# Optimization experiments

Measured on AMD Instinct MI355X. Metric: run time of the kernel, lower is better.

## Reference

```python
import jax, jax.numpy as jnp
import numpy as np

N_EMBD = 768
N_HEAD = 12
HEAD_SIZE = N_EMBD // N_HEAD
LN_EPS = 1e-5


def setup_inputs() -> dict:
    key = jax.random.key(0)
    ks = jax.random.split(key, 12)
    s = 0.02
    B, T, C = 8, 1024, N_EMBD
    return {
        "x":  jax.random.normal(ks[0], (B, T, C), dtype=jnp.float32),
        # per-head q/k/v projections packed as [C, H*hs] (concat of head outputs)
        "Wq": jax.random.normal(ks[1], (C, C), dtype=jnp.float32) * s,
        "Wk": jax.random.normal(ks[2], (C, C), dtype=jnp.float32) * s,
        "Wv": jax.random.normal(ks[3], (C, C), dtype=jnp.float32) * s,
        "Wo": jax.random.normal(ks[4], (C, C), dtype=jnp.float32) * s,
        "bo": jnp.zeros((C,), dtype=jnp.float32),
        "W1": jax.random.normal(ks[5], (C, 4 * C), dtype=jnp.float32) * s,
        "b1": jnp.zeros((4 * C,), dtype=jnp.float32),
        "W2": jax.random.normal(ks[6], (4 * C, C), dtype=jnp.float32) * s,
        "b2": jnp.zeros((C,), dtype=jnp.float32),
        "g1": jnp.ones((C,), dtype=jnp.float32),
        "be1": jnp.zeros((C,), dtype=jnp.float32),
        "g2": jnp.ones((C,), dtype=jnp.float32),
        "be2": jnp.zeros((C,), dtype=jnp.float32),
    }


def _layernorm(x, g, b):
    mu = jnp.mean(x, axis=-1, keepdims=True)
    var = jnp.mean(jnp.square(x - mu), axis=-1, keepdims=True)
    return (x - mu) * jax.lax.rsqrt(var + LN_EPS) * g + b


def _block(x, Wq, Wk, Wv, Wo, bo, W1, b1, W2, b2, g1, be1, g2, be2):
    B, T, C = x.shape
    H, hs = N_HEAD, HEAD_SIZE
    h = _layernorm(x, g1, be1)
    q = (h @ Wq).reshape(B, T, H, hs)
    k = (h @ Wk).reshape(B, T, H, hs)
    v = (h @ Wv).reshape(B, T, H, hs)
    # NOTE: original code scales by n_embd**-0.5 (C from x.shape), not head_size**-0.5
    scores = jnp.einsum("bthd,bshd->bhts", q, k) * (C ** -0.5)
    causal = jnp.tril(jnp.ones((T, T), dtype=bool))  # [T,T]
    scores = jnp.where(causal, scores, -jnp.inf)
    attn = jax.nn.softmax(scores, axis=-1)  # [B,H,T,T]
    o = jnp.einsum("bhts,bshd->bthd", attn, v).reshape(B, T, C)
    x = x + o @ Wo + bo
    h2 = _layernorm(x, g2, be2)
    ff = jax.nn.gelu(h2 @ W1 + b1, approximate=False) @ W2 + b2
    return x + ff


def reference(x, Wq, Wk, Wv, Wo, bo, W1, b1, W2, b2, g1, be1, g2, be2):
    return _block(x, Wq, Wk, Wv, Wo, bo, W1, b1, W2, b2, g1, be1, g2, be2)
```

## Files before the change

kernel.cpp:

```cpp
#include <hip/hip_runtime.h>
#include <math.h>
#include <stdint.h>

typedef unsigned short u16;
typedef unsigned int u32;
typedef __attribute__((ext_vector_type(8))) __bf16 bf16x8;
typedef __attribute__((ext_vector_type(4))) float f32x4;

#define AS1 __attribute__((address_space(1)))
#define AS3 __attribute__((address_space(3)))

__device__ __forceinline__ void stage16(const void* g, void* l) {
    __builtin_amdgcn_global_load_lds((const AS1 void*)(uintptr_t)g,
                                     (AS3 void*)(uintptr_t)l, 16, 0, 0);
}

__device__ __forceinline__ u16 f2bf(float f) {
    u32 u = __float_as_uint(f);
    u += 0x7fffu + ((u >> 16) & 1u);
    return (u16)(u >> 16);
}

__global__ __launch_bounds__(256) void ln_kernel(const float* __restrict__ x,
                                                 const float* __restrict__ g,
                                                 const float* __restrict__ b,
                                                 u16* __restrict__ out) {
    int row = blockIdx.x;
    int tid = threadIdx.x;
    const float* xr = x + (size_t)row * 768;
    float x0 = xr[tid], x1 = xr[tid + 256], x2 = xr[tid + 512];

    __shared__ float red[256];
    red[tid] = x0 + x1 + x2;
    __syncthreads();
    for (int off = 128; off > 0; off >>= 1) {
        if (tid < off) red[tid] += red[tid + off];
        __syncthreads();
    }
    float mu = red[0] * (1.0f / 768.0f);
    __syncthreads();

    float d0 = x0 - mu, d1 = x1 - mu, d2 = x2 - mu;
    red[tid] = d0 * d0 + d1 * d1 + d2 * d2;
    __syncthreads();
    for (int off = 128; off > 0; off >>= 1) {
        if (tid < off) red[tid] += red[tid + off];
        __syncthreads();
    }
    float var = red[0] * (1.0f / 768.0f);
    float rs = rsqrtf(var + 1e-5f);

    u16* orow = out + (size_t)row * 768;
    orow[tid]       = f2bf(d0 * rs * g[tid]       + b[tid]);
    orow[tid + 256] = f2bf(d1 * rs * g[tid + 256] + b[tid + 256]);
    orow[tid + 512] = f2bf(d2 * rs * g[tid + 512] + b[tid + 512]);
}

__global__ __launch_bounds__(256) void transpose_bf16(const float* __restrict__ W,
                                                      u16* __restrict__ Wt,
                                                      int K, int N) {
    __shared__ float t[32][33];
    int tx = threadIdx.x, ty = threadIdx.y;
    int n0 = blockIdx.x * 32, k0 = blockIdx.y * 32;
#pragma unroll
    for (int j = 0; j < 32; j += 8)
        t[ty + j][tx] = W[(size_t)(k0 + ty + j) * N + n0 + tx];
    __syncthreads();
#pragma unroll
    for (int j = 0; j < 32; j += 8)
        Wt[(size_t)(n0 + ty + j) * K + k0 + tx] = f2bf(t[tx][ty + j]);
}

__global__ __launch_bounds__(256) void vt_kernel(const u16* __restrict__ qkv,
                                                 u16* __restrict__ Vt) {
    __shared__ u16 t[32][34];
    const int tx = threadIdx.x, ty = threadIdx.y;
    const int s0 = blockIdx.x * 32, d0 = blockIdx.y * 32, bh = blockIdx.z;
    const int b = bh / 12, h = bh % 12;
#pragma unroll
    for (int j = 0; j < 32; j += 8)
        t[ty + j][tx] = qkv[((size_t)(b * 1024) + s0 + ty + j) * 2304 + 1536 + h * 64 + d0 + tx];
    __syncthreads();
#pragma unroll
    for (int j = 0; j < 32; j += 8)
        Vt[((size_t)bh * 64 + d0 + ty + j) * 1024 + s0 + tx] = t[tx][ty + j];
}

__global__ __launch_bounds__(256, 3) void gemm_k32(
    const u16* __restrict__ A, const u16* __restrict__ Bt,
    const float* __restrict__ bias, const float* __restrict__ res,
    float* __restrict__ outF, u16* __restrict__ outB,
    int N, int K, int act) {
    __shared__ char lds[49152];
    const int tid = threadIdx.x, lane = tid & 63, wid = tid >> 6;
    const int l15 = lane & 15, lk = lane >> 4;
    const int wrow = (wid >> 1) * 64, wcol = (wid & 1) * 64;

    int wg = blockIdx.y * gridDim.x + blockIdx.x;
    const int nwg = gridDim.x * gridDim.y;
    wg = (wg & 7) * (nwg >> 3) + (wg >> 3);
    const int brow = (wg / gridDim.x) * 128;
    const int bcol = (wg % gridDim.x) * 128;

    const size_t K2 = (size_t)K * 2;
    const char* Abase = (const char*)A + (size_t)brow * K2;
    const char* Bbase = (const char*)Bt + (size_t)bcol * K2;

    int srow[2], scol[2];
#pragma unroll
    for (int j = 0; j < 2; ++j) {
        const int L = j * 4096 + tid * 16;
        srow[j] = L >> 6;
        scol[j] = (L & 63) ^ (((srow[j] >> 1) & 3) << 4);
    }

    const int nt = K >> 5;

    auto stage_tile = [&](int t, char* dst) {
#pragma unroll
        for (int j = 0; j < 2; ++j) {
            const size_t off = (size_t)srow[j] * K2 + (size_t)t * 64 + scol[j];
            stage16(Abase + off, dst + j * 4096 + tid * 16);
            stage16(Bbase + off, dst + 8192 + j * 4096 + tid * 16);
        }
    };

    f32x4 acc[4][4] = {};

    stage_tile(0, lds);
    stage_tile(1, lds + 16384);

    for (int t = 0; t < nt; ++t) {
        if (t + 1 < nt) asm volatile("s_waitcnt vmcnt(4)\n\ts_barrier" ::: "memory");
        else            asm volatile("s_waitcnt vmcnt(0)\n\ts_barrier" ::: "memory");
        __builtin_amdgcn_sched_barrier(0);

        if (t + 2 < nt) stage_tile(t + 2, lds + ((t + 2) % 3) * 16384);

        const char* As = lds + (t % 3) * 16384;
        const char* Bs = As + 8192;
        bf16x8 af[4], bfv[4];
#pragma unroll
        for (int m = 0; m < 4; ++m) {
            const int row = wrow + m * 16 + l15;
            af[m] = *(const bf16x8*)(As + row * 64 +
                                     ((lk * 16) ^ (((row >> 1) & 3) << 4)));
        }
#pragma unroll
        for (int n = 0; n < 4; ++n) {
            const int row = wcol + n * 16 + l15;
            bfv[n] = *(const bf16x8*)(Bs + row * 64 +
                                      ((lk * 16) ^ (((row >> 1) & 3) << 4)));
        }
        __builtin_amdgcn_s_setprio(1);
#pragma unroll
        for (int m = 0; m < 4; ++m)
#pragma unroll
            for (int n = 0; n < 4; ++n)
                acc[m][n] = __builtin_amdgcn_mfma_f32_16x16x32_bf16(af[m], bfv[n], acc[m][n], 0, 0, 0);
        __builtin_amdgcn_s_setprio(0);
    }

#pragma unroll
    for (int m = 0; m < 4; ++m)
#pragma unroll
        for (int n = 0; n < 4; ++n)
#pragma unroll
            for (int r = 0; r < 4; ++r) {
                int row = brow + wrow + m * 16 + lk * 4 + r;
                int col = bcol + wcol + n * 16 + l15;
                float v = acc[m][n][r];
                if (bias) v += bias[col];
                if (act) v = 0.5f * v * (1.0f + erff(v * 0.70710678118654752f));
                if (res) v += res[(size_t)row * N + col];
                if (outB) outB[(size_t)row * N + col] = f2bf(v);
                else outF[(size_t)row * N + col] = v;
            }
}

__global__ __launch_bounds__(256) void attn_mfma(const u16* __restrict__ qkv,
                                                 const u16* __restrict__ Vt,
                                                 u16* __restrict__ obf) {
    __shared__ char lds[40960];
    const int tid = threadIdx.x, lane = tid & 63, w = tid >> 6;
    const int g = lane >> 4, l15 = lane & 15;

    int wg = blockIdx.y * gridDim.x + blockIdx.x;
    const int nwg = gridDim.x * gridDim.y;
    wg = (wg & 7) * (nwg >> 3) + (wg >> 3);
    const int qb = 15 - (wg & 15);
    const int bh = wg >> 4;
    const int h = bh % 12, b = bh / 12;
    const int t0 = qb * 64;
    const float scale = 0.03608439182435161f;

    const size_t qrow = ((size_t)b * 1024 + t0 + 16 * w + l15) * 2304 + h * 64;
    const bf16x8 qf0 = *(const bf16x8*)(qkv + qrow + 8 * g);
    const bf16x8 qf1 = *(const bf16x8*)(qkv + qrow + 8 * g + 32);

    const int sub = ((lane & 7) * 16) ^ ((lane >> 3) << 4);
    const int r0 = 16 * w + (lane >> 3);
    const char* kSrc = (const char*)qkv + ((size_t)(b * 1024 + r0) * 2304 + 768 + h * 64) * 2 + sub;
    const char* vSrc = (const char*)Vt + ((size_t)(bh * 64 + r0) * 1024) * 2 + sub;
    const int dstOff = 2 * w * 1024 + lane * 16;

    stage16(kSrc,            lds + dstOff);
    stage16(kSrc + 8 * 4608, lds + dstOff + 1024);
    stage16(vSrc,            lds + 8192 + dstOff);
    stage16(vSrc + 8 * 2048, lds + 8192 + dstOff + 1024);
    kSrc += 64 * 4608; vSrc += 128;
    __syncthreads();

    const int swzA = (l15 & 7) << 4;
    float m_r[4] = {-1e30f, -1e30f, -1e30f, -1e30f};
    float l_r[4] = {0.f, 0.f, 0.f, 0.f};
    f32x4 oacc[4] = {};
    char* Pw = lds + 32768 + w * 2048;

    for (int c = 0; c <= qb; ++c) {
        if (c < qb) {
            char* dst = lds + ((c + 1) & 1) * 16384;
            stage16(kSrc,            dst + dstOff);
            stage16(kSrc + 8 * 4608, dst + dstOff + 1024);
            stage16(vSrc,            dst + 8192 + dstOff);
            stage16(vSrc + 8 * 2048, dst + 8192 + dstOff + 1024);
            kSrc += 64 * 4608; vSrc += 128;
            asm volatile("s_waitcnt vmcnt(4)\n\ts_barrier" ::: "memory");
        } else {
            asm volatile("s_waitcnt vmcnt(0)\n\ts_barrier" ::: "memory");
        }
        __builtin_amdgcn_sched_barrier(0);

        const char* bufK = lds + (c & 1) * 16384;
        const char* bufV = bufK + 8192;

        f32x4 sacc[4] = {};
#pragma unroll
        for (int st = 0; st < 4; ++st) {
            const char* krow = bufK + (l15 + 16 * st) * 128;
            const bf16x8 kf0 = *(const bf16x8*)(krow + ((16 * g) ^ swzA));
            const bf16x8 kf1 = *(const bf16x8*)(krow + ((16 * g + 64) ^ swzA));
            sacc[st] = __builtin_amdgcn_mfma_f32_16x16x32_bf16(qf0, kf0, sacc[st], 0, 0, 0);
            sacc[st] = __builtin_amdgcn_mfma_f32_16x16x32_bf16(qf1, kf1, sacc[st], 0, 0, 0);
        }

        const bool diag = (c == qb);
#pragma unroll
        for (int r = 0; r < 4; ++r) {
            float sv0 = sacc[0][r] * scale, sv1 = sacc[1][r] * scale;
            float sv2 = sacc[2][r] * scale, sv3 = sacc[3][r] * scale;
            if (diag) {
                const int trel = 16 * w + 4 * g + r;
                if (l15 +  0 > trel) sv0 = -1e30f;
                if (l15 + 16 > trel) sv1 = -1e30f;
                if (l15 + 32 > trel) sv2 = -1e30f;
                if (l15 + 48 > trel) sv3 = -1e30f;
            }
            float mx = fmaxf(fmaxf(sv0, sv1), fmaxf(sv2, sv3));
#pragma unroll
            for (int off = 1; off < 16; off <<= 1) mx = fmaxf(mx, __shfl_xor(mx, off));
            const float mnew = fmaxf(m_r[r], mx);
            const float corr = __expf(m_r[r] - mnew);
            const float p0 = __expf(sv0 - mnew), p1 = __expf(sv1 - mnew);
            const float p2 = __expf(sv2 - mnew), p3 = __expf(sv3 - mnew);
            float ps = p0 + p1 + p2 + p3;
#pragma unroll
            for (int off = 1; off < 16; off <<= 1) ps += __shfl_xor(ps, off);
            l_r[r] = l_r[r] * corr + ps;
            m_r[r] = mnew;
            oacc[0][r] *= corr; oacc[1][r] *= corr;
            oacc[2][r] *= corr; oacc[3][r] *= corr;
            const int q = 4 * g + r;
            char* pr = Pw + q * 128;
            const int sw = (q & 7) << 4;
            *(u16*)(pr + ((l15 * 2 +  0) ^ sw)) = f2bf(p0);
            *(u16*)(pr + ((l15 * 2 + 32) ^ sw)) = f2bf(p1);
            *(u16*)(pr + ((l15 * 2 + 64) ^ sw)) = f2bf(p2);
            *(u16*)(pr + ((l15 * 2 + 96) ^ sw)) = f2bf(p3);
        }

#pragma unroll
        for (int kc = 0; kc < 2; ++kc) {
            const bf16x8 pa = *(const bf16x8*)(Pw + l15 * 128 + ((16 * g + 64 * kc) ^ swzA));
#pragma unroll
            for (int dt = 0; dt < 4; ++dt) {
                const int d = l15 + 16 * dt;
                const bf16x8 vf = *(const bf16x8*)(bufV + d * 128 +
                                   ((16 * g + 64 * kc) ^ ((d & 7) << 4)));
                oacc[dt] = __builtin_amdgcn_mfma_f32_16x16x32_bf16(pa, vf, oacc[dt], 0, 0, 0);
            }
        }
        asm volatile("s_barrier" ::: "memory");
    }

    const size_t orow0 = ((size_t)b * 1024 + t0 + 16 * w) * 768 + h * 64;
#pragma unroll
    for (int r = 0; r < 4; ++r) {
        const float inv = 1.0f / l_r[r];
        const size_t orow = orow0 + (size_t)(4 * g + r) * 768;
#pragma unroll
        for (int dt = 0; dt < 4; ++dt)
            obf[orow + 16 * dt + l15] = f2bf(oacc[dt][r] * inv);
    }
}

extern "C" void kernel_launch(void* const* d_in, const int* in_sizes, int n_in,
                              void* d_out, int out_size, void* d_ws, size_t ws_size,
                              hipStream_t stream) {
    const float* x   = (const float*)d_in[0];
    const float* Wq  = (const float*)d_in[1];
    const float* Wk  = (const float*)d_in[2];
    const float* Wv  = (const float*)d_in[3];
    const float* Wo  = (const float*)d_in[4];
    const float* bo  = (const float*)d_in[5];
    const float* W1  = (const float*)d_in[6];
    const float* b1  = (const float*)d_in[7];
    const float* W2  = (const float*)d_in[8];
    const float* b2  = (const float*)d_in[9];
    const float* g1  = (const float*)d_in[10];
    const float* be1 = (const float*)d_in[11];
    const float* g2  = (const float*)d_in[12];
    const float* be2 = (const float*)d_in[13];
    float* out = (float*)d_out;

    char* ws = (char*)d_ws;
    u16* qkv_bf = (u16*)(ws);
    u16* ff1_bf = (u16*)(ws);
    float* x2   = (float*)(ws + 50331648);
    u16* h_bf   = (u16*)(ws + 75497472);
    u16* o_bf   = (u16*)(ws + 88080384);
    u16* Wqkvt  = (u16*)(ws + 100663296);
    u16* W1t    = (u16*)(ws + 104202240);
    u16* W2t    = (u16*)(ws + 108920832);
    u16* Wot    = (u16*)(ws + 113639424);
    u16* Vt     = (u16*)(ws + 114819072);

    dim3 tb(32, 8);
    transpose_bf16<<<dim3(24, 24), tb, 0, stream>>>(Wq, Wqkvt, 768, 768);
    transpose_bf16<<<dim3(24, 24), tb, 0, stream>>>(Wk, Wqkvt + 768 * 768, 768, 768);
    transpose_bf16<<<dim3(24, 24), tb, 0, stream>>>(Wv, Wqkvt + 2 * 768 * 768, 768, 768);
    transpose_bf16<<<dim3(24, 24), tb, 0, stream>>>(Wo, Wot, 768, 768);
    transpose_bf16<<<dim3(96, 24), tb, 0, stream>>>(W1, W1t, 768, 3072);
    transpose_bf16<<<dim3(24, 96), tb, 0, stream>>>(W2, W2t, 3072, 768);

    ln_kernel<<<8192, 256, 0, stream>>>(x, g1, be1, h_bf);
    gemm_k32<<<dim3(18, 64), 256, 0, stream>>>(h_bf, Wqkvt, nullptr, nullptr, nullptr, qkv_bf, 2304, 768, 0);
    vt_kernel<<<dim3(32, 2, 96), tb, 0, stream>>>(qkv_bf, Vt);
    attn_mfma<<<dim3(16, 96), 256, 0, stream>>>(qkv_bf, Vt, o_bf);
    gemm_k32<<<dim3(6, 64), 256, 0, stream>>>(o_bf, Wot, bo, x, x2, nullptr, 768, 768, 0);
    ln_kernel<<<8192, 256, 0, stream>>>(x2, g2, be2, h_bf);
    gemm_k32<<<dim3(24, 64), 256, 0, stream>>>(h_bf, W1t, b1, nullptr, nullptr, ff1_bf, 3072, 768, 1);
    gemm_k32<<<dim3(6, 64), 256, 0, stream>>>(ff1_bf, W2t, b2, x2, out, nullptr, 768, 3072, 0);
}
```

Baseline: 373.9 us.

## Use wave-shuffle LayerNorm, batch weight transposes, unroll GEMM ring, skip redundant rescale

LayerNorm now reduces with wavefront shuffles and a small shared array, replacing the shared-memory tree and its many barriers. The four 768x768 weight transposes are merged into a single launch. The GEMM K-loop is unrolled by three with fixed LDS buffer pointers, which removes the modulo address arithmetic. In attention, the online-softmax rescale is skipped when the running max does not increase. The GEMM unroll assumes the number of K tiles is a multiple of three, which holds for K=768 and K=3072 (24 and 96 tiles).

```diff
diff --git a/kernel.cpp b/kernel.cpp
--- a/kernel.cpp
+++ b/kernel.cpp
@@ -25,29 +25,27 @@
                                                  const float* __restrict__ g,
                                                  const float* __restrict__ b,
                                                  u16* __restrict__ out) {
+    __shared__ float s8[8];
     int row = blockIdx.x;
     int tid = threadIdx.x;
+    const int w = tid >> 6;
     const float* xr = x + (size_t)row * 768;
     float x0 = xr[tid], x1 = xr[tid + 256], x2 = xr[tid + 512];
 
-    __shared__ float red[256];
-    red[tid] = x0 + x1 + x2;
-    __syncthreads();
-    for (int off = 128; off > 0; off >>= 1) {
-        if (tid < off) red[tid] += red[tid + off];
-        __syncthreads();
-    }
-    float mu = red[0] * (1.0f / 768.0f);
-    __syncthreads();
+    float sum = x0 + x1 + x2;
+#pragma unroll
+    for (int off = 32; off; off >>= 1) sum += __shfl_xor(sum, off);
+    if ((tid & 63) == 0) s8[w] = sum;
+    __syncthreads();
+    float mu = (s8[0] + s8[1] + s8[2] + s8[3]) * (1.0f / 768.0f);
 
     float d0 = x0 - mu, d1 = x1 - mu, d2 = x2 - mu;
-    red[tid] = d0 * d0 + d1 * d1 + d2 * d2;
-    __syncthreads();
-    for (int off = 128; off > 0; off >>= 1) {
-        if (tid < off) red[tid] += red[tid + off];
-        __syncthreads();
-    }
-    float var = red[0] * (1.0f / 768.0f);
+    float sq = d0 * d0 + d1 * d1 + d2 * d2;
+#pragma unroll
+    for (int off = 32; off; off >>= 1) sq += __shfl_xor(sq, off);
+    if ((tid & 63) == 0) s8[4 + w] = sq;
+    __syncthreads();
+    float var = (s8[4] + s8[5] + s8[6] + s8[7]) * (1.0f / 768.0f);
     float rs = rsqrtf(var + 1e-5f);
 
     u16* orow = out + (size_t)row * 768;
@@ -69,6 +67,27 @@
 #pragma unroll
     for (int j = 0; j < 32; j += 8)
         Wt[(size_t)(n0 + ty + j) * K + k0 + tx] = f2bf(t[tx][ty + j]);
+}
+
+__global__ __launch_bounds__(256) void transpose4_768(const float* __restrict__ Wq,
+                                                      const float* __restrict__ Wk,
+                                                      const float* __restrict__ Wv,
+                                                      const float* __restrict__ Wo,
+                                                      u16* __restrict__ Wqkvt,
+                                                      u16* __restrict__ Wot) {
+    __shared__ float t[32][33];
+    const int z = blockIdx.z;
+    const float* W = (z == 0) ? Wq : (z == 1) ? Wk : (z == 2) ? Wv : Wo;
+    u16* Wt = (z == 3) ? Wot : (Wqkvt + (size_t)z * 768 * 768);
+    int tx = threadIdx.x, ty = threadIdx.y;
+    int n0 = blockIdx.x * 32, k0 = blockIdx.y * 32;
+#pragma unroll
+    for (int j = 0; j < 32; j += 8)
+        t[ty + j][tx] = W[(size_t)(k0 + ty + j) * 768 + n0 + tx];
+    __syncthreads();
+#pragma unroll
+    for (int j = 0; j < 32; j += 8)
+        Wt[(size_t)(n0 + ty + j) * 768 + k0 + tx] = f2bf(t[tx][ty + j]);
 }
 
 __global__ __launch_bounds__(256) void vt_kernel(const u16* __restrict__ qkv,
@@ -130,15 +149,15 @@
     stage_tile(0, lds);
     stage_tile(1, lds + 16384);
 
-    for (int t = 0; t < nt; ++t) {
+    auto iter = [&](int t, char* buf, char* nxt) {
         if (t + 1 < nt) asm volatile("s_waitcnt vmcnt(4)\n\ts_barrier" ::: "memory");
         else            asm volatile("s_waitcnt vmcnt(0)\n\ts_barrier" ::: "memory");
         __builtin_amdgcn_sched_barrier(0);
 
-        if (t + 2 < nt) stage_tile(t + 2, lds + ((t + 2) % 3) * 16384);
-
-        const char* As = lds + (t % 3) * 16384;
-        const char* Bs = As + 8192;
+        if (t + 2 < nt) stage_tile(t + 2, nxt);
+
+        const char* As = buf;
+        const char* Bs = buf + 8192;
         bf16x8 af[4], bfv[4];
 #pragma unroll
         for (int m = 0; m < 4; ++m) {
@@ -159,6 +178,12 @@
             for (int n = 0; n < 4; ++n)
                 acc[m][n] = __builtin_amdgcn_mfma_f32_16x16x32_bf16(af[m], bfv[n], acc[m][n], 0, 0, 0);
         __builtin_amdgcn_s_setprio(0);
+    };
+
+    for (int t = 0; t < nt; t += 3) {
+        iter(t,     lds,         lds + 32768);
+        iter(t + 1, lds + 16384, lds);
+        iter(t + 2, lds + 32768, lds + 16384);
     }
 
 #pragma unroll
@@ -259,17 +284,19 @@
             float mx = fmaxf(fmaxf(sv0, sv1), fmaxf(sv2, sv3));
 #pragma unroll
             for (int off = 1; off < 16; off <<= 1) mx = fmaxf(mx, __shfl_xor(mx, off));
-            const float mnew = fmaxf(m_r[r], mx);
-            const float corr = __expf(m_r[r] - mnew);
-            const float p0 = __expf(sv0 - mnew), p1 = __expf(sv1 - mnew);
-            const float p2 = __expf(sv2 - mnew), p3 = __expf(sv3 - mnew);
+            if (mx > m_r[r]) {
+                const float corr = __expf(m_r[r] - mx);
+                m_r[r] = mx;
+                l_r[r] *= corr;
+                oacc[0][r] *= corr; oacc[1][r] *= corr;
+                oacc[2][r] *= corr; oacc[3][r] *= corr;
+            }
+            const float p0 = __expf(sv0 - m_r[r]), p1 = __expf(sv1 - m_r[r]);
+            const float p2 = __expf(sv2 - m_r[r]), p3 = __expf(sv3 - m_r[r]);
             float ps = p0 + p1 + p2 + p3;
 #pragma unroll
             for (int off = 1; off < 16; off <<= 1) ps += __shfl_xor(ps, off);
-            l_r[r] = l_r[r] * corr + ps;
-            m_r[r] = mnew;
-            oacc[0][r] *= corr; oacc[1][r] *= corr;
-            oacc[2][r] *= corr; oacc[3][r] *= corr;
+            l_r[r] += ps;
             const int q = 4 * g + r;
             char* pr = Pw + q * 128;
             const int sw = (q & 7) << 4;
@@ -336,10 +363,7 @@
     u16* Vt     = (u16*)(ws + 114819072);
 
     dim3 tb(32, 8);
-    transpose_bf16<<<dim3(24, 24), tb, 0, stream>>>(Wq, Wqkvt, 768, 768);
-    transpose_bf16<<<dim3(24, 24), tb, 0, stream>>>(Wk, Wqkvt + 768 * 768, 768, 768);
-    transpose_bf16<<<dim3(24, 24), tb, 0, stream>>>(Wv, Wqkvt + 2 * 768 * 768, 768, 768);
-    transpose_bf16<<<dim3(24, 24), tb, 0, stream>>>(Wo, Wot, 768, 768);
+    transpose4_768<<<dim3(24, 24, 4), tb, 0, stream>>>(Wq, Wk, Wv, Wo, Wqkvt, Wot);
     transpose_bf16<<<dim3(96, 24), tb, 0, stream>>>(W1, W1t, 768, 3072);
     transpose_bf16<<<dim3(24, 96), tb, 0, stream>>>(W2, W2t, 3072, 768);
 
```

New measurement: 370.2 us. No clear change (-1.0%).
